# Kernel optimization log

Measured on AMD Instinct MI355X. Metric: run time of the kernel, lower is better.

## Reference

```python
import jax, jax.numpy as jnp
import numpy as np

B, S, D = 8, 4096, 1024
C = D // 4          # bottleneck width (downsize=4)
P = 64              # num_prompt_tokens
EPS = 1e-5          # BatchNorm1d eps


def setup_inputs() -> dict:
    key = jax.random.key(0)
    ks = jax.random.split(key, 5)
    return {
        "hidden_states": jax.random.normal(ks[0], (B, S, D), dtype=jnp.float32),
        "W_down": jax.random.normal(ks[1], (C, D), dtype=jnp.float32) / np.sqrt(D),
        "b_down": jax.random.normal(ks[2], (C,), dtype=jnp.float32) * 0.02,
        "gamma": jnp.ones((C,), dtype=jnp.float32),
        "beta": jnp.zeros((C,), dtype=jnp.float32),
        "W_up": jax.random.normal(ks[3], (D, C), dtype=jnp.float32) / np.sqrt(C),
        "b_up": jax.random.normal(ks[4], (D,), dtype=jnp.float32) * 0.02,
    }


def reference(hidden_states, W_down, b_down, gamma, beta, W_up, b_up):
    # proj_down: [B,S,D] -> [B,S,C]
    h = jnp.einsum("bsd,cd->bsc", hidden_states, W_down) + b_down
    b, s, c = h.shape
    win = s // P  # S is a multiple of P, so AdaptiveMaxPool1d == windowed max
    # adaptive max pool over the sequence dim: [B,S,C] -> [B,P,C]
    h = h.reshape(b, P, win, c).max(axis=2)
    h = jax.nn.relu(h)
    # BatchNorm1d over channel dim (training mode: batch stats over B and P)
    mean = h.mean(axis=(0, 1))
    var = ((h - mean) ** 2).mean(axis=(0, 1))  # biased variance, as in BN
    h = (h - mean) * jax.lax.rsqrt(var + EPS) * gamma + beta
    # proj_up: [B,P,C] -> [B,P,D]
    return jnp.einsum("bpc,dc->bpd", h, W_up) + b_up
```

## Files before the change

kernel.cpp:

```cpp
#include <hip/hip_runtime.h>

#define D_  1024
#define C_  256

using bf16x8 = __attribute__((ext_vector_type(8))) __bf16;
using f32x4  = __attribute__((ext_vector_type(4))) float;

__device__ __forceinline__ unsigned short f2bf(float x) {
  unsigned int u = __float_as_uint(x);
  u += 0x7fffu + ((u >> 16) & 1u);
  return (unsigned short)(u >> 16);
}

typedef __attribute__((address_space(1))) const void* gas_t;
typedef __attribute__((address_space(3))) void* las_t;
__device__ __forceinline__ void dma16(const void* g, void* l) {
  __builtin_amdgcn_global_load_lds((gas_t)g, (las_t)l, 16, 0, 0);
}

__global__ void k_prep(const float* __restrict__ wdown, const float* __restrict__ wup,
                       unsigned short* __restrict__ wdb, float* __restrict__ wupT,
                       float* __restrict__ gsum, float* __restrict__ gsq) {
  int bid = blockIdx.x, tid = threadIdx.x;
  if (bid < 256) {
    int idx = (bid * 256 + tid) * 4;
    float4 v = *(const float4*)(wdown + idx);
    int ch = idx >> 10;
    int d  = idx & 1023;
    int kt = d >> 6;
    int c  = d & 63;
    ushort4 o;
    o.x = f2bf(v.x); o.y = f2bf(v.y); o.z = f2bf(v.z); o.w = f2bf(v.w);
    int dstbyte = kt * 32768 + ch * 128 + ((c * 2) ^ ((ch & 7) << 4));
    *(ushort4*)((char*)wdb + dstbyte) = o;
  } else if (bid < 320) {
    __shared__ float t[64][68];
    int b2 = bid - 256;
    int d0 = (b2 >> 2) * 64, c0 = (b2 & 3) * 64;
    #pragma unroll
    for (int r = 0; r < 4; ++r) {
      int idx = r * 256 + tid;
      int dr = idx >> 4, c4 = idx & 15;
      float4 v = *(const float4*)(wup + (d0 + dr) * C_ + c0 + c4 * 4);
      t[dr][c4*4+0] = v.x; t[dr][c4*4+1] = v.y; t[dr][c4*4+2] = v.z; t[dr][c4*4+3] = v.w;
    }
    __syncthreads();
    #pragma unroll
    for (int r = 0; r < 4; ++r) {
      int idx = r * 256 + tid;
      int cr = idx >> 4, d4 = idx & 15;
      float4 v;
      v.x = t[d4*4+0][cr]; v.y = t[d4*4+1][cr]; v.z = t[d4*4+2][cr]; v.w = t[d4*4+3][cr];
      *(float4*)(wupT + (c0 + cr) * D_ + d0 + d4 * 4) = v;
    }
  } else {
    gsum[tid] = 0.f;
    gsq[tid]  = 0.f;
  }
}

__global__ __launch_bounds__(256, 2)
void k_down_pool(const float* __restrict__ hid, const unsigned short* __restrict__ wdb,
                 const float* __restrict__ bdown, float* __restrict__ pooled,
                 float* __restrict__ gsum, float* __restrict__ gsq) {
  __shared__ unsigned short sA0[4096], sA1[4096];
  __shared__ unsigned short sB0[16384], sB1[16384];
  const int bp   = blockIdx.x;
  const int tid  = threadIdx.x;
  const int lane = tid & 63;
  const int wv   = tid >> 6;
  const int l15  = lane & 15;
  const int lg   = lane >> 4;

  const float* hbase = hid + (size_t)bp * 64 * D_;

  f32x4 acc[4][4] = {};
  float4 areg[4];

  auto issueB = [&](unsigned short* sB, int kt) {
    const char* src = (const char*)wdb + kt * 32768;
    #pragma unroll
    for (int i = 0; i < 8; ++i) {
      int off = (i * 4 + wv) * 1024 + lane * 16;
      dma16(src + off, (char*)sB + off);
    }
  };
  auto loadA = [&](int kt) {
    #pragma unroll
    for (int i = 0; i < 4; ++i) {
      int idx = i * 256 + tid;
      int row = idx >> 4, c4 = idx & 15;
      areg[i] = *(const float4*)(hbase + row * D_ + kt * 64 + c4 * 4);
    }
  };
  auto writeA = [&](unsigned short* sA) {
    #pragma unroll
    for (int i = 0; i < 4; ++i) {
      int idx = i * 256 + tid;
      int row = idx >> 4, c4 = idx & 15;
      ushort4 h;
      h.x = f2bf(areg[i].x); h.y = f2bf(areg[i].y); h.z = f2bf(areg[i].z); h.w = f2bf(areg[i].w);
      int off = row * 128 + ((c4 * 8) ^ ((row & 7) << 4));
      *(ushort4*)((char*)sA + off) = h;
    }
  };
  auto compute = [&](const unsigned short* sA, const unsigned short* sB) {
    #pragma unroll
    for (int ks = 0; ks < 2; ++ks) {
      bf16x8 afr[4], bfr[4];
      #pragma unroll
      for (int m = 0; m < 4; ++m) {
        int row = m * 16 + l15;
        int off = row * 128 + ((ks * 64 + lg * 16) ^ ((row & 7) << 4));
        union { uint4 u; bf16x8 v; } t;
        t.u = *(const uint4*)((const char*)sA + off);
        afr[m] = t.v;
      }
      #pragma unroll
      for (int n = 0; n < 4; ++n) {
        int row = wv * 64 + n * 16 + l15;
        int off = row * 128 + ((ks * 64 + lg * 16) ^ ((row & 7) << 4));
        union { uint4 u; bf16x8 v; } t;
        t.u = *(const uint4*)((const char*)sB + off);
        bfr[n] = t.v;
      }
      #pragma unroll
      for (int m = 0; m < 4; ++m)
        #pragma unroll
        for (int n = 0; n < 4; ++n)
          acc[m][n] = __builtin_amdgcn_mfma_f32_16x16x32_bf16(afr[m], bfr[n], acc[m][n], 0, 0, 0);
    }
  };

  loadA(0);
  __builtin_amdgcn_sched_barrier(0);
  issueB(sB0, 0);
  __builtin_amdgcn_sched_barrier(0);
  asm volatile("s_waitcnt vmcnt(8)" ::: "memory");
  writeA(sA0);
  __builtin_amdgcn_sched_barrier(0);
  loadA(1);
  __builtin_amdgcn_sched_barrier(0);
  issueB(sB1, 1);
  __builtin_amdgcn_sched_barrier(0);
  asm volatile("s_waitcnt vmcnt(12) lgkmcnt(0)" ::: "memory");
  __builtin_amdgcn_s_barrier();

  auto step = [&](int i, unsigned short* curA, unsigned short* curB,
                  unsigned short* nxtA, unsigned short* nxtB) {
    compute(curA, curB);
    if (i + 1 < 16) {
      asm volatile("s_waitcnt vmcnt(8)" ::: "memory");
      writeA(nxtA);
    }
    asm volatile("s_waitcnt lgkmcnt(0)" ::: "memory");
    __builtin_amdgcn_s_barrier();
    if (i + 2 < 16) {
      loadA(i + 2);
      __builtin_amdgcn_sched_barrier(0);
      issueB(curB, i + 2);
      __builtin_amdgcn_sched_barrier(0);
      asm volatile("s_waitcnt vmcnt(12)" ::: "memory");
    } else {
      asm volatile("s_waitcnt vmcnt(0)" ::: "memory");
    }
    __builtin_amdgcn_s_barrier();
  };

  #pragma unroll 1
  for (int kt = 0; kt < 16; kt += 2) {
    step(kt,     sA0, sB0, sA1, sB1);
    step(kt + 1, sA1, sB1, sA0, sB0);
  }

  #pragma unroll
  for (int n = 0; n < 4; ++n) {
    float vmax = -__builtin_inff();
    #pragma unroll
    for (int m = 0; m < 4; ++m)
      #pragma unroll
      for (int r = 0; r < 4; ++r)
        vmax = fmaxf(vmax, acc[m][n][r]);
    vmax = fmaxf(vmax, __shfl_xor(vmax, 16, 64));
    vmax = fmaxf(vmax, __shfl_xor(vmax, 32, 64));
    int col = wv * 64 + n * 16 + l15;
    if (lane < 16) {
      float pv = fmaxf(vmax + bdown[col], 0.f);
      pooled[bp * C_ + col] = pv;
      atomicAdd(&gsum[col], pv);
      atomicAdd(&gsq[col],  pv * pv);
    }
  }
}

__global__ __launch_bounds__(256)
void k_up(const float* __restrict__ pooled, const float* __restrict__ wupT,
          const float* __restrict__ gsum, const float* __restrict__ gsq,
          const float* __restrict__ gamma, const float* __restrict__ beta,
          const float* __restrict__ bup, float* __restrict__ out) {
  __shared__ float sx0[256], sx1[256];
  int tid = threadIdx.x;
  int r0 = blockIdx.x * 2;
  float mean = gsum[tid] * (1.f / 512.f);
  float var  = gsq[tid] * (1.f / 512.f) - mean * mean;
  float inv  = 1.f / sqrtf(var + 1e-5f);
  float sc = gamma[tid] * inv;
  float sh = beta[tid] - mean * sc;
  sx0[tid] = pooled[r0 * C_ + tid] * sc + sh;
  sx1[tid] = pooled[(r0 + 1) * C_ + tid] * sc + sh;
  __syncthreads();
  int d4 = tid * 4;
  float a0=0,a1=0,a2=0,a3=0,b0=0,b1=0,b2=0,b3=0;
  #pragma unroll 8
  for (int k = 0; k < 256; ++k) {
    float4 w = *(const float4*)(wupT + (size_t)k * D_ + d4);
    float x0 = sx0[k], x1 = sx1[k];
    a0 += w.x * x0; a1 += w.y * x0; a2 += w.z * x0; a3 += w.w * x0;
    b0 += w.x * x1; b1 += w.y * x1; b2 += w.z * x1; b3 += w.w * x1;
  }
  float4 bb = *(const float4*)(bup + d4);
  float4 o0 = {a0 + bb.x, a1 + bb.y, a2 + bb.z, a3 + bb.w};
  float4 o1 = {b0 + bb.x, b1 + bb.y, b2 + bb.z, b3 + bb.w};
  *(float4*)(out + (size_t)r0 * D_ + d4) = o0;
  *(float4*)(out + (size_t)(r0 + 1) * D_ + d4) = o1;
}

extern "C" void kernel_launch(void* const* d_in, const int* in_sizes, int n_in,
                              void* d_out, int out_size, void* d_ws, size_t ws_size,
                              hipStream_t stream) {
  const float* hid   = (const float*)d_in[0];
  const float* wdown = (const float*)d_in[1];
  const float* bdown = (const float*)d_in[2];
  const float* gamma = (const float*)d_in[3];
  const float* beta  = (const float*)d_in[4];
  const float* wup   = (const float*)d_in[5];
  const float* bup   = (const float*)d_in[6];
  float* out = (float*)d_out;

  char* ws = (char*)d_ws;
  unsigned short* wdb = (unsigned short*)ws;
  float* wupT   = (float*)(ws + (512 << 10));
  float* pooled = (float*)(ws + (1536 << 10));
  float* gsum   = (float*)(ws + (2048 << 10));
  float* gsq    = (float*)(ws + (2048 << 10) + 1024);

  hipLaunchKernelGGL(k_prep,      dim3(321), dim3(256), 0, stream, wdown, wup, wdb, wupT, gsum, gsq);
  hipLaunchKernelGGL(k_down_pool, dim3(512), dim3(256), 0, stream, hid, wdb, bdown, pooled, gsum, gsq);
  hipLaunchKernelGGL(k_up,        dim3(256), dim3(256), 0, stream, pooled, wupT, gsum, gsq, gamma, beta, bup, out);
}
```

Baseline: 240.3 us.

## Load W_down fragments directly from global in MFMA layout, drop LDS B staging

The prep kernel now stores the bf16 W_down in a per-lane MFMA fragment order. The GEMM reads B fragments straight from global/L2 into registers instead of DMA-staging 32KB tiles into LDS, which frees 64KB of LDS and simplifies the pipeline to a plain double-buffered A with syncthreads. The up-projection kernel is also re-tiled so each block computes 8 rows by 256 columns, reusing each W_up load across 8 rows. The risk is higher global/L2 traffic and exposed latency on the B loads, since the hand-tuned waitcnt pipelining is gone.

```diff
diff --git a/kernel.cpp b/kernel.cpp
--- a/kernel.cpp
+++ b/kernel.cpp
@@ -10,12 +10,6 @@
   unsigned int u = __float_as_uint(x);
   u += 0x7fffu + ((u >> 16) & 1u);
   return (unsigned short)(u >> 16);
-}
-
-typedef __attribute__((address_space(1))) const void* gas_t;
-typedef __attribute__((address_space(3))) void* las_t;
-__device__ __forceinline__ void dma16(const void* g, void* l) {
-  __builtin_amdgcn_global_load_lds((gas_t)g, (las_t)l, 16, 0, 0);
 }
 
 __global__ void k_prep(const float* __restrict__ wdown, const float* __restrict__ wup,
@@ -28,11 +22,15 @@
     int ch = idx >> 10;
     int d  = idx & 1023;
     int kt = d >> 6;
-    int c  = d & 63;
+    int ks = (d >> 5) & 1;
+    int lg = (d >> 3) & 3;
+    int j0 = d & 7;
+    int lane = lg * 16 + (ch & 15);
+    int grp  = (kt * 16 + (ch >> 4)) * 2 + ks;
     ushort4 o;
     o.x = f2bf(v.x); o.y = f2bf(v.y); o.z = f2bf(v.z); o.w = f2bf(v.w);
-    int dstbyte = kt * 32768 + ch * 128 + ((c * 2) ^ ((ch & 7) << 4));
-    *(ushort4*)((char*)wdb + dstbyte) = o;
+    size_t byteoff = ((size_t)grp * 64 + lane) * 16 + j0 * 2;
+    *(ushort4*)((char*)wdb + byteoff) = o;
   } else if (bid < 320) {
     __shared__ float t[64][68];
     int b2 = bid - 256;
@@ -64,7 +62,6 @@
                  const float* __restrict__ bdown, float* __restrict__ pooled,
                  float* __restrict__ gsum, float* __restrict__ gsq) {
   __shared__ unsigned short sA0[4096], sA1[4096];
-  __shared__ unsigned short sB0[16384], sB1[16384];
   const int bp   = blockIdx.x;
   const int tid  = threadIdx.x;
   const int lane = tid & 63;
@@ -77,14 +74,6 @@
   f32x4 acc[4][4] = {};
   float4 areg[4];
 
-  auto issueB = [&](unsigned short* sB, int kt) {
-    const char* src = (const char*)wdb + kt * 32768;
-    #pragma unroll
-    for (int i = 0; i < 8; ++i) {
-      int off = (i * 4 + wv) * 1024 + lane * 16;
-      dma16(src + off, (char*)sB + off);
-    }
-  };
   auto loadA = [&](int kt) {
     #pragma unroll
     for (int i = 0; i < 4; ++i) {
@@ -104,10 +93,15 @@
       *(ushort4*)((char*)sA + off) = h;
     }
   };
-  auto compute = [&](const unsigned short* sA, const unsigned short* sB) {
+  auto compute = [&](const unsigned short* sA, int kt) {
+    const char* wb = (const char*)wdb + ((size_t)(kt * 32 + wv * 8) << 10) + lane * 16;
     #pragma unroll
     for (int ks = 0; ks < 2; ++ks) {
-      bf16x8 afr[4], bfr[4];
+      union { uint4 u; bf16x8 v; } b[4];
+      #pragma unroll
+      for (int n = 0; n < 4; ++n)
+        b[n].u = *(const uint4*)(wb + ((n * 2 + ks) << 10));
+      bf16x8 afr[4];
       #pragma unroll
       for (int m = 0; m < 4; ++m) {
         int row = m * 16 + l15;
@@ -117,60 +111,25 @@
         afr[m] = t.v;
       }
       #pragma unroll
-      for (int n = 0; n < 4; ++n) {
-        int row = wv * 64 + n * 16 + l15;
-        int off = row * 128 + ((ks * 64 + lg * 16) ^ ((row & 7) << 4));
-        union { uint4 u; bf16x8 v; } t;
-        t.u = *(const uint4*)((const char*)sB + off);
-        bfr[n] = t.v;
-      }
-      #pragma unroll
-      for (int m = 0; m < 4; ++m)
+      for (int n = 0; n < 4; ++n)
         #pragma unroll
-        for (int n = 0; n < 4; ++n)
-          acc[m][n] = __builtin_amdgcn_mfma_f32_16x16x32_bf16(afr[m], bfr[n], acc[m][n], 0, 0, 0);
+        for (int m = 0; m < 4; ++m)
+          acc[m][n] = __builtin_amdgcn_mfma_f32_16x16x32_bf16(afr[m], b[n].v, acc[m][n], 0, 0, 0);
     }
   };
 
   loadA(0);
-  __builtin_amdgcn_sched_barrier(0);
-  issueB(sB0, 0);
-  __builtin_amdgcn_sched_barrier(0);
-  asm volatile("s_waitcnt vmcnt(8)" ::: "memory");
   writeA(sA0);
-  __builtin_amdgcn_sched_barrier(0);
-  loadA(1);
-  __builtin_amdgcn_sched_barrier(0);
-  issueB(sB1, 1);
-  __builtin_amdgcn_sched_barrier(0);
-  asm volatile("s_waitcnt vmcnt(12) lgkmcnt(0)" ::: "memory");
-  __builtin_amdgcn_s_barrier();
-
-  auto step = [&](int i, unsigned short* curA, unsigned short* curB,
-                  unsigned short* nxtA, unsigned short* nxtB) {
-    compute(curA, curB);
-    if (i + 1 < 16) {
-      asm volatile("s_waitcnt vmcnt(8)" ::: "memory");
-      writeA(nxtA);
-    }
-    asm volatile("s_waitcnt lgkmcnt(0)" ::: "memory");
-    __builtin_amdgcn_s_barrier();
-    if (i + 2 < 16) {
-      loadA(i + 2);
-      __builtin_amdgcn_sched_barrier(0);
-      issueB(curB, i + 2);
-      __builtin_amdgcn_sched_barrier(0);
-      asm volatile("s_waitcnt vmcnt(12)" ::: "memory");
-    } else {
-      asm volatile("s_waitcnt vmcnt(0)" ::: "memory");
-    }
-    __builtin_amdgcn_s_barrier();
-  };
+  __syncthreads();
 
   #pragma unroll 1
-  for (int kt = 0; kt < 16; kt += 2) {
-    step(kt,     sA0, sB0, sA1, sB1);
-    step(kt + 1, sA1, sB1, sA0, sB0);
+  for (int kt = 0; kt < 16; ++kt) {
+    unsigned short* cur = (kt & 1) ? sA1 : sA0;
+    unsigned short* nxt = (kt & 1) ? sA0 : sA1;
+    if (kt < 15) loadA(kt + 1);
+    compute(cur, kt);
+    if (kt < 15) writeA(nxt);
+    __syncthreads();
   }
 
   #pragma unroll
@@ -198,31 +157,31 @@
           const float* __restrict__ gsum, const float* __restrict__ gsq,
           const float* __restrict__ gamma, const float* __restrict__ beta,
           const float* __restrict__ bup, float* __restrict__ out) {
-  __shared__ float sx0[256], sx1[256];
+  __shared__ float sx[8][256];
   int tid = threadIdx.x;
-  int r0 = blockIdx.x * 2;
+  int dg = blockIdx.x & 3;
+  int r0 = (blockIdx.x >> 2) * 8;
   float mean = gsum[tid] * (1.f / 512.f);
   float var  = gsq[tid] * (1.f / 512.f) - mean * mean;
   float inv  = 1.f / sqrtf(var + 1e-5f);
   float sc = gamma[tid] * inv;
   float sh = beta[tid] - mean * sc;
-  sx0[tid] = pooled[r0 * C_ + tid] * sc + sh;
-  sx1[tid] = pooled[(r0 + 1) * C_ + tid] * sc + sh;
+  #pragma unroll
+  for (int r = 0; r < 8; ++r)
+    sx[r][tid] = pooled[(r0 + r) * C_ + tid] * sc + sh;
   __syncthreads();
-  int d4 = tid * 4;
-  float a0=0,a1=0,a2=0,a3=0,b0=0,b1=0,b2=0,b3=0;
-  #pragma unroll 8
+  int d = dg * 256 + tid;
+  float acc[8] = {};
+  #pragma unroll 4
   for (int k = 0; k < 256; ++k) {
-    float4 w = *(const float4*)(wupT + (size_t)k * D_ + d4);
-    float x0 = sx0[k], x1 = sx1[k];
-    a0 += w.x * x0; a1 += w.y * x0; a2 += w.z * x0; a3 += w.w * x0;
-    b0 += w.x * x1; b1 += w.y * x1; b2 += w.z * x1; b3 += w.w * x1;
-  }
-  float4 bb = *(const float4*)(bup + d4);
-  float4 o0 = {a0 + bb.x, a1 + bb.y, a2 + bb.z, a3 + bb.w};
-  float4 o1 = {b0 + bb.x, b1 + bb.y, b2 + bb.z, b3 + bb.w};
-  *(float4*)(out + (size_t)r0 * D_ + d4) = o0;
-  *(float4*)(out + (size_t)(r0 + 1) * D_ + d4) = o1;
+    float w = wupT[(size_t)k * D_ + d];
+    #pragma unroll
+    for (int r = 0; r < 8; ++r) acc[r] += sx[r][k] * w;
+  }
+  float bb = bup[d];
+  #pragma unroll
+  for (int r = 0; r < 8; ++r)
+    out[(size_t)(r0 + r) * D_ + d] = acc[r] + bb;
 }
 
 extern "C" void kernel_launch(void* const* d_in, const int* in_sizes, int n_in,
```

After: 270.5 us. 1.13x slower.
